# Performance work log

Measured on AMD Instinct MI355X. Metric: run time of the kernel, lower is better.

Reference implementation:

```python
import jax, jax.numpy as jnp
import numpy as np
from jax import lax

B, C, L = 2048, 9605, 8
WL_PER_LABEL = 50
ALPHA = 0.5        # training_config['alpha4']
ALPHA1 = 0.1       # margin
ALPHA2 = 2.0       # training_config['alpha2']
ALPHA3 = 10.0      # training_config['alpha3']
ALPHA_OTHER = 0.5
NEG = jnp.float32(-1e30)


def setup_inputs() -> dict:
    key = jax.random.key(0)
    k1, k2, k3, k4 = jax.random.split(key, 4)
    x = jax.random.normal(k1, (B, C), dtype=jnp.float32) * 2.0
    y = (jax.random.uniform(k2, (B, C)) < 0.005).astype(jnp.float32)
    y_neg = (jax.random.uniform(k3, (B, C)) < 0.005).astype(jnp.float32)
    # whitelist masks: L app-labels, each whitelisting ~WL_PER_LABEL raw classes
    idx = jax.random.randint(k4, (L, WL_PER_LABEL), 0, C)
    wl_masks = jnp.zeros((L, C), dtype=bool).at[jnp.arange(L)[:, None], idx].set(True)
    return {"x": x, "y": y, "y_neg": y_neg, "wl_masks": wl_masks}


def reference(x, y, y_neg, wl_masks):
    # y_neg is consumed by the original forward (find_gt_whitelist) but never
    # affects the returned loss, faithfully ignored here.
    xs_pos = jax.nn.sigmoid(x)                                  # [B, C]
    # top_k_thres = max(11th-largest sigmoid, alpha_other)
    thres = jnp.maximum(lax.top_k(xs_pos, 11)[0][:, 10], ALPHA_OTHER)  # [B]
    # per-label whitelist max: m[b,l] = max_{c in wl_l} xs_pos[b,c]
    m = jnp.max(jnp.where(wl_masks[None, :, :], xs_pos[:, None, :], NEG), axis=-1)  # [B, L]
    # label l is a ground-truth whitelist label iff y has any positive in wl_l
    has_pos = jnp.einsum('bc,lc->bl', y, wl_masks.astype(y.dtype)) > 0   # [B, L]
    correct_max = jnp.max(jnp.where(has_pos, m, NEG), axis=-1)           # [B]
    incorrect_max = jnp.max(jnp.where(~has_pos, m, NEG), axis=-1)        # [B]
    any_correct = jnp.any(has_pos, axis=-1)
    any_incorrect = jnp.any(~has_pos, axis=-1)
    # union whitelist max (the "other" branch uses xs_pos over all wl indices)
    union_max = jnp.max(jnp.where(jnp.any(wl_masks, axis=0)[None, :], xs_pos, NEG), axis=-1)
    x1 = jnp.where(any_correct, correct_max, thres)
    x2 = jnp.where(any_correct,
                   jnp.where(any_incorrect, jnp.maximum(incorrect_max, thres), thres),
                   union_max)
    coef = jnp.where(any_correct, 1.0, 1.0 - ALPHA)
    d = x2 - x1 + ALPHA1
    rank = jnp.where(d > 0, ALPHA2, 1.0) * jax.nn.sigmoid(ALPHA3 * d)
    return jnp.mean(coef * rank)
```

## Files before the change

### kernel.cpp

```cpp
#include <hip/hip_runtime.h>

#define CC 9605
#define BB 2048
#define LL 8
#define NEGF (-1e30f)
#define NINF (-__builtin_huge_valf())

#define WS_PARTIALS_OFF 16384

__device__ __forceinline__ unsigned enc_f(float f) {
  unsigned u = __float_as_uint(f);
  return (u & 0x80000000u) ? ~u : (u | 0x80000000u);
}
__device__ __forceinline__ float dec_u(unsigned e) {
  unsigned u = (e & 0x80000000u) ? (e & 0x7fffffffu) : ~e;
  return __uint_as_float(u);
}
__device__ __forceinline__ float sigm(float z) {
  return 1.0f / (1.0f + __expf(-z));
}

__global__ void wl_sniff(const unsigned* __restrict__ wlw,
                         unsigned* __restrict__ wsu) {
  const int nwords = (LL * CC) / 4;
  const int stride = gridDim.x * blockDim.x;
  unsigned f = 0u;
  for (int j = blockIdx.x * blockDim.x + threadIdx.x; j < nwords; j += stride) {
    unsigned w = wlw[j];
#pragma unroll
    for (int k = 0; k < 4; ++k) {
      unsigned b = (w >> (8 * k)) & 255u;
      if (b == 1u)    { f |= 2u; if (k != 0) f |= 1u; }
      if (b == 0x3fu) { f |= 8u; if (k == 1) f |= 4u; }
    }
  }
#pragma unroll
  for (int off = 32; off >= 1; off >>= 1) f |= __shfl_xor(f, off, 64);
  if ((threadIdx.x & 63) == 0 && f) atomicOr(&wsu[1], f);
}

__global__ void wl_compact(const unsigned char* __restrict__ wl,
                           unsigned* __restrict__ wsu) {
  const int tid = threadIdx.x;
  const int lane = tid & 63;
  const int c = blockIdx.x * 256 + tid;
  const unsigned g = wsu[1];
  const int dt = (g & 1u) ? 0 : (g & 4u) ? 3 : (g & 2u) ? 1 : (g & 8u) ? 2 : 0;
  const int* wl32 = (const int*)wl;
  const float* wlf = (const float*)wl;
  const unsigned short* wlh = (const unsigned short*)wl;
  unsigned m = 0u;
  if (c < CC) {
#pragma unroll
    for (int l = 0; l < LL; ++l) {
      int j = l * CC + c;
      bool on;
      if (dt == 0) on = (wl[j] != 0);
      else if (dt == 1) on = (wl32[j] != 0);
      else if (dt == 2) on = (wlf[j] != 0.0f);
      else on = (wlh[j] != 0);
      if (on) m |= (1u << l);
    }
  }
  unsigned long long bal = __ballot(m != 0u);
  if (bal) {
    unsigned wcnt = (unsigned)__popcll(bal);
    unsigned basep = 0u;
    if (lane == 0) basep = atomicAdd(&wsu[0], wcnt);
    basep = __shfl(basep, 0, 64);
    if (m) {
      unsigned pos = basep + (unsigned)__popcll(bal & ((1ull << lane) - 1ull));
      if (pos < 2048u) wsu[4 + pos] = ((unsigned)c << 8) | m;
    }
  }
}


#define FOR11(OP) OP(0) OP(1) OP(2) OP(3) OP(4) OP(5) OP(6) OP(7) OP(8) OP(9) OP(10)
#define FOR11I(OP) OP(0) OP(1) OP(2) OP(3) OP(4) OP(5) OP(6) OP(7) OP(8) OP(9) OP(10)
#define FOR8(OP) OP(0) OP(1) OP(2) OP(3) OP(4) OP(5) OP(6) OP(7)

#define DECL_S(k) float s_##k = NINF;
#define INS1(k) { float _hi = fmaxf(s_##k, cv); cv = fminf(s_##k, cv); s_##k = _hi; }
#define TOP11V(v) { float cv = (v); FOR11I(INS1) }
#define TOP4(T) { TOP11V((T).x) TOP11V((T).y) TOP11V((T).z) TOP11V((T).w) }

__global__ __launch_bounds__(128, 1) void loss_kernel(
    const float* __restrict__ x, const float* __restrict__ y,
    const unsigned* __restrict__ wsu, float* __restrict__ partials) {
  __shared__ float sh_top[64][11];
  __shared__ float sh_w1lm[8];
  __shared__ unsigned sh_w1pm;

  const int tid = threadIdx.x;
  const int lane = tid & 63;
  const int w = tid >> 6;
  const int r = blockIdx.x;
  const long long base = (long long)r * CC;

  const unsigned nu = min(wsu[0], 2048u);
  const unsigned* ents = wsu + 4;

  const int soff = (4 - (r & 3)) & 3;
  const int ng = (CC - soff) >> 2;
  const int rem = ng - 2368;
  const int tailn = CC - soff - (ng << 2);
  const int m_extra = soff + tailn;
  const float4* vp = (const float4*)(x + base + soff);

  FOR11(DECL_S)

  const int g0 = w ? 1216 : 0;
  float4 a0 = vp[g0 + lane];
  float4 a1 = vp[g0 + lane + 64];
  float4 a2 = vp[g0 + lane + 128];
  float4 a3 = vp[g0 + lane + 192];
  int gb = g0 + lane;
#pragma unroll 1
  for (int it = 0; it < 3; ++it) {
    float4 b0 = vp[gb + 256];
    float4 b1 = vp[gb + 320];
    float4 b2 = vp[gb + 384];
    float4 b3 = vp[gb + 448];
    TOP4(a0) TOP4(a1) TOP4(a2) TOP4(a3)
    a0 = b0; a1 = b1; a2 = b2; a3 = b3;
    gb += 256;
  }
  if (w == 0) {
    float4 b0 = vp[gb + 256];
    float4 b1 = vp[gb + 320];
    float4 b2 = vp[gb + 384];
    TOP4(a0) TOP4(a1) TOP4(a2) TOP4(a3)
    TOP4(b0) TOP4(b1) TOP4(b2)
  } else {
    float4 b0 = vp[gb + 256];
    float4 b1 = vp[gb + 320];
    float4 tr = make_float4(NINF, NINF, NINF, NINF);
    if (lane < rem) tr = vp[2368 + lane];
    float tv = NINF;
    if (lane < m_extra) {
      int tc = (lane < soff) ? lane : (soff + (ng << 2) + (lane - soff));
      tv = x[base + tc];
    }
    TOP4(a0) TOP4(a1) TOP4(a2) TOP4(a3)
    TOP4(b0) TOP4(b1) TOP4(tr)
    TOP11V(tv)
  }

  unsigned en0, en1, en2, en3;
  {
    unsigned e0 = (unsigned)lane + 64u * (unsigned)w;
    en0 = (e0 < nu) ? ents[e0] : 0u;
    en1 = (e0 + 128u < nu) ? ents[e0 + 128u] : 0u;
    en2 = (e0 + 256u < nu) ? ents[e0 + 256u] : 0u;
    en3 = (e0 + 384u < nu) ? ents[e0 + 384u] : 0u;
  }
  float gx0 = x[base + (en0 >> 8)], gy0 = y[base + (en0 >> 8)];
  float gx1 = x[base + (en1 >> 8)], gy1 = y[base + (en1 >> 8)];
  float gx2 = x[base + (en2 >> 8)], gy2 = y[base + (en2 >> 8)];
  float gx3 = x[base + (en3 >> 8)], gy3 = y[base + (en3 >> 8)];

#define DECL_LM(k) float lm_##k = NEGF;
  FOR8(DECL_LM)
  unsigned pmask = 0u;
#define FOLDE(EN, GX, GY)                                        \
  {                                                              \
    unsigned mk = (EN) & 255u;    \
    pmask |= mk;                                                 \
    if ((GY) > 0.0f) pmask |= (mk << 8);                         \
    if (mk & 1u)   lm_0 = fmaxf(lm_0, (GX));                     \
    if (mk & 2u)   lm_1 = fmaxf(lm_1, (GX));                     \
    if (mk & 4u)   lm_2 = fmaxf(lm_2, (GX));                     \
    if (mk & 8u)   lm_3 = fmaxf(lm_3, (GX));                     \
    if (mk & 16u)  lm_4 = fmaxf(lm_4, (GX));                     \
    if (mk & 32u)  lm_5 = fmaxf(lm_5, (GX));                     \
    if (mk & 64u)  lm_6 = fmaxf(lm_6, (GX));                     \
    if (mk & 128u) lm_7 = fmaxf(lm_7, (GX));                     \
  }
  FOLDE(en0, gx0, gy0)
  FOLDE(en1, gx1, gy1)
  FOLDE(en2, gx2, gy2)
  FOLDE(en3, gx3, gy3)
  for (unsigned e = 512u + (unsigned)tid; e < nu; e += 128u) {
    unsigned ent = ents[e];
    float xv = x[base + (ent >> 8)];
    float yv = y[base + (ent >> 8)];
    FOLDE(ent, xv, yv)
  }
#pragma unroll
  for (int off = 32; off >= 1; off >>= 1) {
    pmask |= __shfl_xor(pmask, off, 64);
#define RED1(l) lm_##l = fmaxf(lm_##l, __shfl_xor(lm_##l, off, 64));
    FOR8(RED1)
#undef RED1
  }

  if (w == 1) {
#define ST1(k) sh_top[lane][k] = s_##k;
    FOR11(ST1)
#undef ST1
    if (lane == 0) {
#define STL(l) sh_w1lm[l] = lm_##l;
      FOR8(STL)
#undef STL
      sh_w1pm = pmask;
    }
  }
  __syncthreads();
  if (w != 0) return;

#define MG1(k) TOP11V(sh_top[lane][k])
  FOR11(MG1)
#undef MG1

#define DECL_E(k) unsigned e_##k = enc_f(s_##k);
  FOR11(DECL_E)
#undef DECL_E
  unsigned wlo = e_10;
  unsigned whi = e_0;
#pragma unroll
  for (int off = 32; off >= 1; off >>= 1) {
    wlo = max(wlo, __shfl_xor(wlo, off, 64));
    whi = max(whi, __shfl_xor(whi, off, 64));
  }
  unsigned lo = wlo, hi = whi + 1u;
  while (hi - lo > 1u) {
    unsigned mid = lo + ((hi - lo) >> 1);
    unsigned cnt = 0u;
#define CMP1(k) cnt += (e_##k >= mid) ? 1u : 0u;
    FOR11(CMP1)
#undef CMP1
    unsigned tot = (unsigned)__popcll(__ballot(cnt & 1u)) +
                   ((unsigned)__popcll(__ballot(cnt & 2u)) << 1) +
                   ((unsigned)__popcll(__ballot(cnt & 4u)) << 2) +
                   ((unsigned)__popcll(__ballot(cnt & 8u)) << 3);
    if (tot >= 11u) lo = mid; else hi = mid;
  }
  const unsigned E11 = lo;

  if (lane == 0) {
    pmask |= sh_w1pm;
#define CMB(l) lm_##l = fmaxf(lm_##l, sh_w1lm[l]);
    FOR8(CMB)
#undef CMB
    unsigned PR = pmask & 255u, PO = (pmask >> 8) & 255u;
    float thres = fmaxf(sigm(dec_u(E11)), 0.5f);
    float cmax = NEGF, imax = NEGF, umax = NEGF;
#define EP1(l)                                                   \
    if ((PR >> l) & 1u) {                                        \
      float ml = sigm(lm_##l);                                   \
      umax = fmaxf(umax, ml);                                    \
      if ((PO >> l) & 1u) cmax = fmaxf(cmax, ml);                \
      else imax = fmaxf(imax, ml);                               \
    }
    FOR8(EP1)
#undef EP1
    bool anyc = (PO != 0u);
    bool anyi = (PO != 255u);
    float x1 = anyc ? cmax : thres;
    float x2 = anyc ? (anyi ? fmaxf(imax, thres) : thres)
                    : ((nu > 0u) ? umax : NEGF);
    float coef = anyc ? 1.0f : 0.5f;
    float dd = x2 - x1 + 0.1f;
    float rank = ((dd > 0.0f) ? 2.0f : 1.0f) * sigm(10.0f * dd);
    partials[r] = coef * rank;
  }
}

__global__ void final_reduce(const float* __restrict__ partials,
                             float* __restrict__ out) {
  __shared__ float sh[4];
  const int tid = threadIdx.x;
  const int lane = tid & 63;
  const int wid = tid >> 6;
  float s = 0.0f;
  for (int i = tid; i < BB; i += 256) s += partials[i];
#pragma unroll
  for (int off = 32; off >= 1; off >>= 1) s += __shfl_xor(s, off, 64);
  if (lane == 0) sh[wid] = s;
  __syncthreads();
  if (tid == 0) out[0] = (sh[0] + sh[1] + sh[2] + sh[3]) * (1.0f / (float)BB);
}

extern "C" void kernel_launch(void* const* d_in, const int* in_sizes, int n_in,
                              void* d_out, int out_size, void* d_ws,
                              size_t ws_size, hipStream_t stream) {
  const float* x = (const float*)d_in[0];
  const float* y = (const float*)d_in[1];
  const unsigned char* wl = (const unsigned char*)d_in[3];
  float* out = (float*)d_out;
  unsigned* wsu = (unsigned*)d_ws;
  float* partials = (float*)((char*)d_ws + WS_PARTIALS_OFF);

  hipMemsetAsync(d_ws, 0, 16, stream);
  wl_sniff<<<64, 256, 0, stream>>>((const unsigned*)wl, wsu);
  wl_compact<<<(CC + 255) / 256, 256, 0, stream>>>(wl, wsu);
  loss_kernel<<<BB, 128, 0, stream>>>(x, y, wsu, partials);
  final_reduce<<<1, 256, 0, stream>>>(partials, out);
}
```

Measured before the change: 222.9 us.

## Split per-row top-11 scan across four wavefronts per block

The loss kernel moves from 128 to 256 threads per row, so each of four wavefronts scans about 600 float4 groups instead of roughly 1200. Partial top-11 lists from waves 1-3 are merged in wave 0 through shared memory, and the whitelist gather is redistributed over 256 threads. The aim is more parallelism per row and shorter serial insertion chains, which should hide memory latency better. In exchange, wave 0 does a longer serial merge (33 extra insertions), the per-wave load pipelining is gone, and the (128,1) launch-bounds hint is removed.

```diff
diff --git a/kernel.cpp b/kernel.cpp
--- a/kernel.cpp
+++ b/kernel.cpp
@@ -85,12 +85,12 @@
 #define TOP11V(v) { float cv = (v); FOR11I(INS1) }
 #define TOP4(T) { TOP11V((T).x) TOP11V((T).y) TOP11V((T).z) TOP11V((T).w) }
 
-__global__ __launch_bounds__(128, 1) void loss_kernel(
+__global__ __launch_bounds__(256) void loss_kernel(
     const float* __restrict__ x, const float* __restrict__ y,
     const unsigned* __restrict__ wsu, float* __restrict__ partials) {
-  __shared__ float sh_top[64][11];
-  __shared__ float sh_w1lm[8];
-  __shared__ unsigned sh_w1pm;
+  __shared__ float sh_top[3][64][11];
+  __shared__ float sh_wlm[4][8];
+  __shared__ unsigned sh_wpm[4];
 
   const int tid = threadIdx.x;
   const int lane = tid & 63;
@@ -103,62 +103,41 @@
 
   const int soff = (4 - (r & 3)) & 3;
   const int ng = (CC - soff) >> 2;
-  const int rem = ng - 2368;
   const int tailn = CC - soff - (ng << 2);
   const int m_extra = soff + tailn;
   const float4* vp = (const float4*)(x + base + soff);
 
   FOR11(DECL_S)
 
-  const int g0 = w ? 1216 : 0;
-  float4 a0 = vp[g0 + lane];
-  float4 a1 = vp[g0 + lane + 64];
-  float4 a2 = vp[g0 + lane + 128];
-  float4 a3 = vp[g0 + lane + 192];
-  int gb = g0 + lane;
-#pragma unroll 1
-  for (int it = 0; it < 3; ++it) {
-    float4 b0 = vp[gb + 256];
-    float4 b1 = vp[gb + 320];
-    float4 b2 = vp[gb + 384];
-    float4 b3 = vp[gb + 448];
-    TOP4(a0) TOP4(a1) TOP4(a2) TOP4(a3)
-    a0 = b0; a1 = b1; a2 = b2; a3 = b3;
-    gb += 256;
-  }
-  if (w == 0) {
-    float4 b0 = vp[gb + 256];
-    float4 b1 = vp[gb + 320];
-    float4 b2 = vp[gb + 384];
-    TOP4(a0) TOP4(a1) TOP4(a2) TOP4(a3)
-    TOP4(b0) TOP4(b1) TOP4(b2)
-  } else {
-    float4 b0 = vp[gb + 256];
-    float4 b1 = vp[gb + 320];
-    float4 tr = make_float4(NINF, NINF, NINF, NINF);
-    if (lane < rem) tr = vp[2368 + lane];
+  const int g0 = 600 * w + lane;
+#pragma unroll
+  for (int k = 0; k < 9; ++k) {
+    float4 t = vp[g0 + 64 * k];
+    TOP4(t)
+  }
+  {
+    float4 t = make_float4(NINF, NINF, NINF, NINF);
+    if (lane < 24) t = vp[600 * w + 576 + lane];
+    TOP4(t)
+  }
+  if (w == 3) {
+    {
+      float4 t = make_float4(NINF, NINF, NINF, NINF);
+      if (2400 + lane < ng) t = vp[2400 + lane];
+      TOP4(t)
+    }
     float tv = NINF;
     if (lane < m_extra) {
       int tc = (lane < soff) ? lane : (soff + (ng << 2) + (lane - soff));
       tv = x[base + tc];
     }
-    TOP4(a0) TOP4(a1) TOP4(a2) TOP4(a3)
-    TOP4(b0) TOP4(b1) TOP4(tr)
     TOP11V(tv)
   }
 
-  unsigned en0, en1, en2, en3;
-  {
-    unsigned e0 = (unsigned)lane + 64u * (unsigned)w;
-    en0 = (e0 < nu) ? ents[e0] : 0u;
-    en1 = (e0 + 128u < nu) ? ents[e0 + 128u] : 0u;
-    en2 = (e0 + 256u < nu) ? ents[e0 + 256u] : 0u;
-    en3 = (e0 + 384u < nu) ? ents[e0 + 384u] : 0u;
-  }
+  unsigned en0 = ((unsigned)tid < nu) ? ents[tid] : 0u;
+  unsigned en1 = ((unsigned)tid + 256u < nu) ? ents[tid + 256] : 0u;
   float gx0 = x[base + (en0 >> 8)], gy0 = y[base + (en0 >> 8)];
   float gx1 = x[base + (en1 >> 8)], gy1 = y[base + (en1 >> 8)];
-  float gx2 = x[base + (en2 >> 8)], gy2 = y[base + (en2 >> 8)];
-  float gx3 = x[base + (en3 >> 8)], gy3 = y[base + (en3 >> 8)];
 
 #define DECL_LM(k) float lm_##k = NEGF;
   FOR8(DECL_LM)
@@ -179,9 +158,7 @@
   }
   FOLDE(en0, gx0, gy0)
   FOLDE(en1, gx1, gy1)
-  FOLDE(en2, gx2, gy2)
-  FOLDE(en3, gx3, gy3)
-  for (unsigned e = 512u + (unsigned)tid; e < nu; e += 128u) {
+  for (unsigned e = 512u + (unsigned)tid; e < nu; e += 256u) {
     unsigned ent = ents[e];
     float xv = x[base + (ent >> 8)];
     float yv = y[base + (ent >> 8)];
@@ -195,23 +172,27 @@
 #undef RED1
   }
 
-  if (w == 1) {
-#define ST1(k) sh_top[lane][k] = s_##k;
+  if (w > 0) {
+#define ST1(k) sh_top[w - 1][lane][k] = s_##k;
     FOR11(ST1)
 #undef ST1
-    if (lane == 0) {
-#define STL(l) sh_w1lm[l] = lm_##l;
-      FOR8(STL)
+  }
+  if (lane == 0) {
+#define STL(l) sh_wlm[w][l] = lm_##l;
+    FOR8(STL)
 #undef STL
-      sh_w1pm = pmask;
-    }
+    sh_wpm[w] = pmask;
   }
   __syncthreads();
   if (w != 0) return;
 
-#define MG1(k) TOP11V(sh_top[lane][k])
-  FOR11(MG1)
-#undef MG1
+#pragma unroll
+  for (int j = 0; j < 3; ++j) {
+#pragma unroll
+    for (int k = 0; k < 11; ++k) {
+      TOP11V(sh_top[j][lane][k])
+    }
+  }
 
 #define DECL_E(k) unsigned e_##k = enc_f(s_##k);
   FOR11(DECL_E)
@@ -239,10 +220,13 @@
   const unsigned E11 = lo;
 
   if (lane == 0) {
-    pmask |= sh_w1pm;
-#define CMB(l) lm_##l = fmaxf(lm_##l, sh_w1lm[l]);
-    FOR8(CMB)
+#pragma unroll
+    for (int j = 1; j < 4; ++j) {
+      pmask |= sh_wpm[j];
+#define CMB(l) lm_##l = fmaxf(lm_##l, sh_wlm[j][l]);
+      FOR8(CMB)
 #undef CMB
+    }
     unsigned PR = pmask & 255u, PO = (pmask >> 8) & 255u;
     float thres = fmaxf(sigm(dec_u(E11)), 0.5f);
     float cmax = NEGF, imax = NEGF, umax = NEGF;
@@ -295,6 +279,6 @@
   hipMemsetAsync(d_ws, 0, 16, stream);
   wl_sniff<<<64, 256, 0, stream>>>((const unsigned*)wl, wsu);
   wl_compact<<<(CC + 255) / 256, 256, 0, stream>>>(wl, wsu);
-  loss_kernel<<<BB, 128, 0, stream>>>(x, y, wsu, partials);
+  loss_kernel<<<BB, 256, 0, stream>>>(x, y, wsu, partials);
   final_reduce<<<1, 256, 0, stream>>>(partials, out);
 }
```

New measurement: 222.2 us. No clear change (-0.3%).
